# Kernel optimization log

Measured on AMD Instinct MI355X. Metric: run time of the kernel, lower is better.

The kernel has to match this reference:

```python
import jax, jax.numpy as jnp
import numpy as np

D = 100  # embedding_dim (hard-coded in the original module)


def _prelu(x, a):
    return jnp.where(x >= 0, x, a * x)


def setup_inputs() -> dict:
    key = jax.random.key(0)
    ks = jax.random.split(key, 12)
    B, S, L, R, V = 32, 50, 20, 16, 50000
    T = L * R  # tokens per sentence = len_max_sentence * n_routes
    return {
        "stories": jax.random.randint(ks[0], (B, S, T), 0, V),
        "queries": jax.random.randint(ks[1], (B, L), 0, V),
        "emb": 0.1 * jax.random.normal(ks[2], (V, D), dtype=jnp.float32),
        "in_mult": jnp.ones((T, D), dtype=jnp.float32),
        "q_mult": jnp.ones((L, D), dtype=jnp.float32),
        "keys": 0.1 * jax.random.normal(ks[3], (R, D), dtype=jnp.float32),
        "init_state": 0.1 * jax.random.normal(ks[4], (D,), dtype=jnp.float32),
        "U": 0.1 * jax.random.normal(ks[5], (R * D, D), dtype=jnp.float32),
        "Vw": 0.1 * jax.random.normal(ks[6], (R * D, R * D), dtype=jnp.float32),
        "Ww": 0.1 * jax.random.normal(ks[7], (R * D, R * D), dtype=jnp.float32),
        "Hw": 0.1 * jax.random.normal(ks[8], (D, D), dtype=jnp.float32),
        "Rw": 0.1 * jax.random.normal(ks[9], (V, D), dtype=jnp.float32),
        "alpha_in": jnp.ones((1,), dtype=jnp.float32),  # PReLU(init=1)
        "alpha_q": jnp.ones((1,), dtype=jnp.float32),
    }


def reference(stories, queries, emb, in_mult, q_mult, keys, init_state,
              U, Vw, Ww, Hw, Rw, alpha_in, alpha_q):
    B, S, T = stories.shape
    R = keys.shape[0]
    emb0 = emb.at[0].set(0.0)  # padding_idx=0 row is zero
    # stories -> [B,S,T,D] -> route-sum -> [B,S,R,D]
    x = emb0[stories] * in_mult
    x = x.reshape(B, S, R, T // R, D).sum(axis=3)
    # V(keys.flatten()) is constant across timesteps
    v_keys = (keys.reshape(-1) @ Vw.T).reshape(R, D)
    state0 = jnp.tile(init_state[None, None, :], (B, 1, 1))  # [B,1,D]

    def step(state, sent):  # state [B,1,D], sent [B,R,D]
        gate = jax.nn.sigmoid(sent * state + sent * keys)
        u = (state.reshape(B, D) @ U.T).reshape(B, R, D)
        w = (sent.reshape(B, R * D) @ Ww.T).reshape(B, R, D)
        cand = _prelu(u + v_keys + w, alpha_in)
        # null-sentence mask: zero out positions where gate == sigmoid(0) = 0.5
        mask = jax.lax.stop_gradient(jnp.where(gate == 0.5, 0.0, 1.0))
        state = state + (cand * gate * mask).sum(axis=1, keepdims=True)
        # torch.norm over singleton dim=1 (= elementwise abs), kept faithful
        state = state / jnp.sqrt(jnp.sum(state * state, axis=1, keepdims=True))
        return state, None

    state, _ = jax.lax.scan(step, state0, jnp.swapaxes(x, 0, 1))

    q = (emb0[queries] * q_mult).sum(axis=1, keepdims=True)  # [B,1,D]
    h = _prelu(q + (state.reshape(B, D) @ Hw.T).reshape(B, 1, D), alpha_q)
    return h.reshape(B, D) @ Rw.T  # [B, vocab]
```

## Files before the change

kernel.cpp:

```cpp
#include <hip/hip_runtime.h>
#include <cstddef>
#include <cstdint>

#define B_  32
#define S_  50
#define L_  20
#define R_  16
#define D_  100
#define V_  50000
#define T_  320
#define RD_ 1600
#define BS_ 1600
#define NG_ 25
#define NP_ 16

typedef float v4f __attribute__((ext_vector_type(4)));
typedef unsigned v2u __attribute__((ext_vector_type(2)));
typedef unsigned short u16;
#define NTL(p)  __builtin_nontemporal_load((const v4f*)(p))
#define NTL8(p) __builtin_nontemporal_load((const v2u*)(p))

__device__ __forceinline__ float uf(unsigned u) { return __uint_as_float(u); }

__device__ __forceinline__ void bsplit(float a, unsigned& h, unsigned& l) {
  const unsigned bits = __float_as_uint(a);
  const unsigned hb = bits & 0xffff0000u;
  h = hb >> 16;
  l = __float_as_uint(a - __uint_as_float(hb)) >> 16;
}

__global__ __launch_bounds__(512) void setup_kernel(
    const int* __restrict__ stories, const float* __restrict__ emb,
    const float* __restrict__ in_mult, const float* __restrict__ U,
    const float* __restrict__ Vw, const float* __restrict__ keys,
    const float* __restrict__ init_state, const float* __restrict__ Ww,
    u16* __restrict__ xh, u16* __restrict__ xl,
    u16* __restrict__ wh, u16* __restrict__ wl,
    float* __restrict__ table, float* __restrict__ vk, float* __restrict__ u0)
{
  const int blk = blockIdx.x, tid = threadIdx.x;
  if (blk < 1600) {
    __shared__ int toks[T_];
    const int* st = stories + (size_t)blk * T_;
    if (tid < T_) toks[tid] = st[tid];
    __syncthreads();
    if (tid < 400) {
      const int j4 = tid * 4;
      const int r  = j4 / D_;
      const int d4 = j4 - r * D_;
      float4 acc = make_float4(0.f, 0.f, 0.f, 0.f);
      #pragma unroll
      for (int l = 0; l < 20; ++l) {
        const int t = r * 20 + l;
        const int tok = toks[t];
        if (tok != 0) {
          float4 e = *(const float4*)&emb[(size_t)tok * D_ + d4];
          float4 m = *(const float4*)&in_mult[(size_t)t * D_ + d4];
          acc.x += e.x * m.x; acc.y += e.y * m.y;
          acc.z += e.z * m.z; acc.w += e.w * m.w;
        }
      }
      unsigned h0,h1,h2,h3,l0,l1,l2,l3;
      bsplit(acc.x, h0, l0); bsplit(acc.y, h1, l1);
      bsplit(acc.z, h2, l2); bsplit(acc.w, h3, l3);
      v2u hv, lv;
      hv.x = h0 | (h1 << 16); hv.y = h2 | (h3 << 16);
      lv.x = l0 | (l1 << 16); lv.y = l2 | (l3 << 16);
      *(v2u*)&xh[(size_t)blk * RD_ + j4] = hv;
      *(v2u*)&xl[(size_t)blk * RD_ + j4] = lv;
    }
  } else if (blk < 2000) {
    const int q = blk - 1600;
    const int g = q >> 4, p = q & 15;
    const float s0 = (p & 1) ? -1.f : 1.f;
    const float s1 = (p & 2) ? -1.f : 1.f;
    const float s2 = (p & 4) ? -1.f : 1.f;
    const float s3 = (p & 8) ? -1.f : 1.f;
    if (tid < 400) {
      const int j4 = tid * 4;
      float t[4];
      #pragma unroll
      for (int jj = 0; jj < 4; ++jj) {
        const float* ur = &U[(size_t)(j4 + jj) * D_ + 4 * g];
        t[jj] = s0*ur[0] + s1*ur[1] + s2*ur[2] + s3*ur[3];
      }
      *(float4*)&table[((size_t)(g * NP_ + p)) * RD_ + j4] =
          make_float4(t[0], t[1], t[2], t[3]);
    }
  } else if (blk < 2200) {
    const int wave = tid >> 6, lane = tid & 63;
    const int j = (blk - 2000) * 8 + wave;
    float acc = 0.f;
    for (int k = lane; k < RD_; k += 64)
      acc += keys[k] * Vw[(size_t)j * RD_ + k];
    #pragma unroll
    for (int off = 32; off > 0; off >>= 1) acc += __shfl_down(acc, off);
    if (lane == 0) vk[j] = acc;
  } else if (blk < 2400) {
    const int wave = tid >> 6, lane = tid & 63;
    const int j = (blk - 2200) * 8 + wave;
    const float* Ur = U + (size_t)j * D_;
    float acc = Ur[lane] * init_state[lane];
    if (lane < 36) acc += Ur[64 + lane] * init_state[64 + lane];
    #pragma unroll
    for (int off = 32; off > 0; off >>= 1) acc += __shfl_down(acc, off);
    if (lane == 0) u0[j] = acc;
  } else {
    const int e = ((blk - 2400) * 512 + tid) * 8;
    float4 a0 = *(const float4*)&Ww[e];
    float4 a1 = *(const float4*)&Ww[e + 4];
    unsigned h[8], l[8];
    bsplit(a0.x, h[0], l[0]); bsplit(a0.y, h[1], l[1]);
    bsplit(a0.z, h[2], l[2]); bsplit(a0.w, h[3], l[3]);
    bsplit(a1.x, h[4], l[4]); bsplit(a1.y, h[5], l[5]);
    bsplit(a1.z, h[6], l[6]); bsplit(a1.w, h[7], l[7]);
    uint4 hv = make_uint4(h[0]|(h[1]<<16), h[2]|(h[3]<<16),
                          h[4]|(h[5]<<16), h[6]|(h[7]<<16));
    uint4 lv = make_uint4(l[0]|(l[1]<<16), l[2]|(l[3]<<16),
                          l[4]|(l[5]<<16), l[6]|(l[7]<<16));
    *(uint4*)&wh[e] = hv;
    *(uint4*)&wl[e] = lv;
  }
}

typedef const __attribute__((address_space(1))) unsigned GAu;
typedef __attribute__((address_space(3))) unsigned LDSu;
#define GLL(SRC, DST) __builtin_amdgcn_global_load_lds((GAu*)(SRC), (LDSu*)(DST), 16, 0, 0)

__device__ __forceinline__ void mfma16(v4f& d, v4f a, v4f b) {
  asm("v_mfma_f32_16x16x32_bf16 %0, %1, %2, %0" : "+v"(d) : "v"(a), "v"(b));
}

__global__ __launch_bounds__(256) void gemm_mfma_kernel(
    const u16* __restrict__ xh, const u16* __restrict__ xl,
    const u16* __restrict__ wh, const u16* __restrict__ wl,
    float* __restrict__ C)
{
  __shared__ __align__(16) char smem[2][4][8192];
  const int tid = threadIdx.x;
  const int lane = tid & 63, wid = tid >> 6;
  const int bm = blockIdx.y * 128, bn = blockIdx.x * 128;

  int ldsoff[2], srcA[2], srcB[2];
  #pragma unroll
  for (int i = 0; i < 2; ++i) {
    const int chunk = wid * 2 + i;
    const int row = chunk * 16 + (lane >> 2);
    const int kb = (lane & 3) * 16;
    int ra = bm + row; if (ra > 1599) ra = 1599;
    int rb = bn + row; if (rb > 1599) rb = 1599;
    srcA[i] = ra * 3200 + kb;
    srcB[i] = rb * 3200 + kb;
    ldsoff[i] = chunk * 1024;
  }
  const char* gxh = (const char*)xh;
  const char* gxl = (const char*)xl;
  const char* gwh = (const char*)wh;
  const char* gwl = (const char*)wl;

  const int wm = wid >> 1, wn = wid & 1;
  const int r15 = lane & 15, q = lane >> 4;
  const int aoff = (wm * 64 + r15) * 64 + q * 16;
  const int boff = (wn * 64 + r15) * 64 + q * 16;

  v4f acc[4][4];
  #pragma unroll
  for (int i = 0; i < 4; ++i)
    #pragma unroll
    for (int j = 0; j < 4; ++j) acc[i][j] = (v4f)(0.f);

  auto stage = [&](int buf, int kt) {
    const int kb = kt * 64;
    #pragma unroll
    for (int i = 0; i < 2; ++i) {
      GLL(gxh + srcA[i] + kb, &smem[buf][0][ldsoff[i]]);
      GLL(gxl + srcA[i] + kb, &smem[buf][1][ldsoff[i]]);
      GLL(gwh + srcB[i] + kb, &smem[buf][2][ldsoff[i]]);
      GLL(gwl + srcB[i] + kb, &smem[buf][3][ldsoff[i]]);
    }
  };

  stage(0, 0);
  __syncthreads();

  for (int kt = 0; kt < 50; ++kt) {
    const int cur = kt & 1;
    if (kt < 49) stage(cur ^ 1, kt + 1);
    const char* s0 = &smem[cur][0][0];
    v4f ah[4], al[4], bh[4], bl[4];
    #pragma unroll
    for (int t = 0; t < 4; ++t) {
      ah[t] = *(const v4f*)(s0 +         aoff + t * 1024);
      al[t] = *(const v4f*)(s0 +  8192 + aoff + t * 1024);
      bh[t] = *(const v4f*)(s0 + 16384 + boff + t * 1024);
      bl[t] = *(const v4f*)(s0 + 24576 + boff + t * 1024);
    }
    #pragma unroll
    for (int im = 0; im < 4; ++im)
      #pragma unroll
      for (int in = 0; in < 4; ++in) {
        mfma16(acc[im][in], ah[im], bh[in]);
        mfma16(acc[im][in], ah[im], bl[in]);
        mfma16(acc[im][in], al[im], bh[in]);
      }
    __syncthreads();
  }

  const int mb  = bm + wm * 64 + q * 4;
  const int nbq = bn + wn * 64 + r15;
  #pragma unroll
  for (int im = 0; im < 4; ++im) {
    #pragma unroll
    for (int in = 0; in < 4; ++in) {
      const int n = nbq + in * 16;
      const int m0 = mb + im * 16;
      if (n < 1600) {
        #pragma unroll
        for (int r = 0; r < 4; ++r)
          if (m0 + r < 1600)
            C[(size_t)(m0 + r) * 1600 + n] = acc[im][in][r];
      }
    }
  }
}

__global__ __launch_bounds__(512, 2) void scan_kernel(
    const u16* __restrict__ xh,
    const u16* __restrict__ xl,
    const float* __restrict__ Wall,
    const float* __restrict__ table,
    const float* __restrict__ u0,
    const float* __restrict__ vkeys,
    const float* __restrict__ keys,
    const float* __restrict__ init_state,
    const float* __restrict__ alpha_in_p,
    const int*   __restrict__ queries,
    const float* __restrict__ emb,
    const float* __restrict__ q_mult,
    const float* __restrict__ Hw,
    const float* __restrict__ alpha_q_p,
    float* __restrict__ h_g)
{
  const int b = blockIdx.x, tid = threadIdx.x;
  __shared__ __align__(16) float s_state[D_];
  __shared__ __align__(16) float s_c[RD_];
  __shared__ float s_hw[D_ * 101];
  __shared__ unsigned long long s_mask[2];
  const float alpha = alpha_in_p[0];
  const bool active = (tid < 400);
  const int j4 = tid * 4;
  const int d4 = (j4 % D_);
  float4 kk = make_float4(0.f,0.f,0.f,0.f), vv = kk;
  const u16*   xhb = xh   + (size_t)b * S_ * RD_;
  const u16*   xlb = xl   + (size_t)b * S_ * RD_;
  const float* wb  = Wall + (size_t)b * S_ * RD_;
  v2u bxh[5], bxl[5]; v4f bw[5];
  #pragma unroll
  for (int i = 0; i < 5; ++i) { bxh[i] = (v2u)(0u); bxl[i] = (v2u)(0u); bw[i] = (v4f)(0.f); }
  if (active) {
    kk = *(const float4*)&keys[j4];
    vv = *(const float4*)&vkeys[j4];
    #pragma unroll
    for (int i = 0; i < 5; ++i) {
      bxh[i] = NTL8(&xhb[(size_t)i * RD_ + j4]);
      bxl[i] = NTL8(&xlb[(size_t)i * RD_ + j4]);
      bw[i]  = NTL(&wb[(size_t)i * RD_ + j4]);
    }
  }
  if (tid < D_) s_state[tid] = init_state[tid];
  __syncthreads();

  for (int sg = 0; sg < S_; sg += 5) {
    #pragma unroll
    for (int i = 0; i < 5; ++i) {
      const int s = sg + i;
      if (active) {
        const v2u hxv = bxh[i], lxv = bxl[i];
        const v4f w = bw[i];
        if (s + 5 < S_) {
          bxh[i] = NTL8(&xhb[(size_t)(s + 5) * RD_ + j4]);
          bxl[i] = NTL8(&xlb[(size_t)(s + 5) * RD_ + j4]);
          bw[i]  = NTL(&wb[(size_t)(s + 5) * RD_ + j4]);
        }
        v4f sent;
        sent.x = uf(hxv.x << 16)          + uf(lxv.x << 16);
        sent.y = uf(hxv.x & 0xffff0000u)  + uf(lxv.x & 0xffff0000u);
        sent.z = uf(hxv.y << 16)          + uf(lxv.y << 16);
        sent.w = uf(hxv.y & 0xffff0000u)  + uf(lxv.y & 0xffff0000u);
        v4f u;
        if (s == 0) {
          float4 t0 = *(const float4*)&u0[j4];
          u.x = t0.x; u.y = t0.y; u.z = t0.z; u.w = t0.w;
        } else {
          u = (v4f)(0.f);
          const unsigned long long m0 = s_mask[0];
          const unsigned long long m1 = s_mask[1];
          #pragma unroll
          for (int g = 0; g < NG_; ++g) {
            const unsigned idx = (g < 16)
                ? (unsigned)((m0 >> (4 * g)) & 15ull)
                : (unsigned)((m1 >> (4 * g - 64)) & 15ull);
            float4 tv = *(const float4*)&table[((size_t)(g * NP_) + idx) * RD_ + j4];
            u.x += tv.x; u.y += tv.y; u.z += tv.z; u.w += tv.w;
          }
        }
        float4 sd = *(const float4*)&s_state[d4];
        float zx = sent.x * sd.x + sent.x * kk.x;
        float zy = sent.y * sd.y + sent.y * kk.y;
        float zz = sent.z * sd.z + sent.z * kk.z;
        float zw = sent.w * sd.w + sent.w * kk.w;
        float gx = 1.0f / (1.0f + expf(-zx));
        float gy = 1.0f / (1.0f + expf(-zy));
        float gz = 1.0f / (1.0f + expf(-zz));
        float gw = 1.0f / (1.0f + expf(-zw));
        float cx = u.x + vv.x + w.x; cx = cx >= 0.f ? cx : alpha * cx;
        float cy = u.y + vv.y + w.y; cy = cy >= 0.f ? cy : alpha * cy;
        float cz = u.z + vv.z + w.z; cz = cz >= 0.f ? cz : alpha * cz;
        float cw = u.w + vv.w + w.w; cw = cw >= 0.f ? cw : alpha * cw;
        v4f cc;
        cc.x = (gx == 0.5f) ? 0.f : cx * gx;
        cc.y = (gy == 0.5f) ? 0.f : cy * gy;
        cc.z = (gz == 0.5f) ? 0.f : cz * gz;
        cc.w = (gw == 0.5f) ? 0.f : cw * gw;
        *(v4f*)&s_c[j4] = cc;
      }
      __syncthreads();
      if (tid < D_) {
        float csum = 0.f;
        #pragma unroll
        for (int r = 0; r < R_; ++r) csum += s_c[r * D_ + tid];
        float v = s_state[tid] + csum;
        v = v / sqrtf(v * v);
        s_state[tid] = v;
        unsigned long long mask = __ballot(v < 0.f);
        if ((tid & 63) == 0) s_mask[tid >> 6] = mask;
      }
      __syncthreads();
    }
  }

  for (int f = tid; f < D_ * D_; f += 512) {
    const int row = f / D_, col = f - row * D_;
    s_hw[row * 101 + col] = Hw[f];
  }
  __syncthreads();
  if (tid < D_) {
    float q = 0.f;
    #pragma unroll
    for (int l = 0; l < L_; ++l) {
      const int tok = queries[b * L_ + l];
      if (tok != 0) q += emb[(size_t)tok * D_ + tid] * q_mult[l * D_ + tid];
    }
    float a = 0.f;
    #pragma unroll 4
    for (int k = 0; k < D_; ++k) a += s_state[k] * s_hw[tid * 101 + k];
    float h = q + a;
    const float aq = alpha_q_p[0];
    h = h >= 0.f ? h : aq * h;
    h_g[(size_t)b * D_ + tid] = h;
  }
}

__global__ __launch_bounds__(256) void out_kernel(
    const float* __restrict__ h_g, const float* __restrict__ Rw, float* __restrict__ out)
{
  __shared__ __align__(16) float sh[B_ * D_];
  __shared__ __align__(16) float sr[32 * D_];
  int tid = threadIdx.x;
  int v0 = blockIdx.x * 32;
  for (int i = tid; i < B_ * D_; i += 256) sh[i] = h_g[i];
  int nrows = V_ - v0; if (nrows > 32) nrows = 32;
  for (int i = tid; i < nrows * D_; i += 256) sr[i] = Rw[(size_t)v0 * D_ + i];
  __syncthreads();
  const float4* sh4 = (const float4*)sh;
  const float4* sr4 = (const float4*)sr;
  int tv = (tid & 15) * 2;
  int tb = (tid >> 4) * 2;
  float a00 = 0.f, a01 = 0.f, a10 = 0.f, a11 = 0.f;
  #pragma unroll
  for (int kc = 0; kc < 25; ++kc) {
    float4 h0 = sh4[tb * 25 + kc];
    float4 h1 = sh4[(tb + 1) * 25 + kc];
    float4 r0 = sr4[tv * 25 + kc];
    float4 r1 = sr4[(tv + 1) * 25 + kc];
    a00 += h0.x*r0.x + h0.y*r0.y + h0.z*r0.z + h0.w*r0.w;
    a01 += h0.x*r1.x + h0.y*r1.y + h0.z*r1.z + h0.w*r1.w;
    a10 += h1.x*r0.x + h1.y*r0.y + h1.z*r0.z + h1.w*r0.w;
    a11 += h1.x*r1.x + h1.y*r1.y + h1.z*r1.z + h1.w*r1.w;
  }
  if (tv < nrows) {
    out[(size_t)tb * V_ + v0 + tv] = a00;
    out[(size_t)(tb + 1) * V_ + v0 + tv] = a10;
  }
  if (tv + 1 < nrows) {
    out[(size_t)tb * V_ + v0 + tv + 1] = a01;
    out[(size_t)(tb + 1) * V_ + v0 + tv + 1] = a11;
  }
}

extern "C" void kernel_launch(void* const* d_in, const int* in_sizes, int n_in,
                              void* d_out, int out_size, void* d_ws, size_t ws_size,
                              hipStream_t stream) {
  const int*   stories    = (const int*)  d_in[0];
  const int*   queries    = (const int*)  d_in[1];
  const float* emb        = (const float*)d_in[2];
  const float* in_mult    = (const float*)d_in[3];
  const float* q_mult     = (const float*)d_in[4];
  const float* keys       = (const float*)d_in[5];
  const float* init_state = (const float*)d_in[6];
  const float* U          = (const float*)d_in[7];
  const float* Vw         = (const float*)d_in[8];
  const float* Ww         = (const float*)d_in[9];
  const float* Hw         = (const float*)d_in[10];
  const float* Rw         = (const float*)d_in[11];
  const float* alpha_in   = (const float*)d_in[12];
  const float* alpha_q    = (const float*)d_in[13];
  float* out = (float*)d_out;

  char* ws = (char*)d_ws;
  u16*   xh    = (u16*)  (ws);
  u16*   xl    = (u16*)  (ws +  5120000);
  float* Wall  = (float*)(ws + 10240000);
  float* table = (float*)(ws + 20480000);
  u16*   wwh   = (u16*)  (ws + 23040000);
  u16*   wwl   = (u16*)  (ws + 28160000);
  float* vk    = (float*)(ws + 33280000);
  float* u0    = (float*)(ws + 33286400);
  float* hbuf  = (float*)(ws + 33292800);

  setup_kernel<<<3025, 512, 0, stream>>>(stories, emb, in_mult, U, Vw, keys,
                                         init_state, Ww, xh, xl, wwh, wwl,
                                         table, vk, u0);
  gemm_mfma_kernel<<<dim3(13, 13), 256, 0, stream>>>(xh, xl, wwh, wwl, Wall);
  scan_kernel<<<B_, 512, 0, stream>>>(xh, xl, Wall, table, u0, vk, keys,
                                      init_state, alpha_in, queries, emb,
                                      q_mult, Hw, alpha_q, hbuf);
  out_kernel<<<(V_ + 31) / 32, 256, 0, stream>>>(hbuf, Rw, out);
}
```

Before: 419.0 us.

## Store story sums as fp32 and split to bf16 hi/lo inside GEMM staging

The setup kernel now writes the route-summed story embeddings as plain fp32 instead of pre-split bf16 high/low arrays. The GEMM loads A through registers and does the bf16 split itself while filling shared memory, overlapping that with the MFMA work, and the scan kernel reads fp32 sentences directly with no reconstruction. This removes one workspace write and read pair and the unpack arithmetic in the serial scan, at the cost of register-path A staging in the GEMM in place of direct global-to-LDS loads.

```diff
diff --git a/kernel.cpp b/kernel.cpp
--- a/kernel.cpp
+++ b/kernel.cpp
@@ -15,10 +15,8 @@
 #define NP_ 16
 
 typedef float v4f __attribute__((ext_vector_type(4)));
-typedef unsigned v2u __attribute__((ext_vector_type(2)));
 typedef unsigned short u16;
 #define NTL(p)  __builtin_nontemporal_load((const v4f*)(p))
-#define NTL8(p) __builtin_nontemporal_load((const v2u*)(p))
 
 __device__ __forceinline__ float uf(unsigned u) { return __uint_as_float(u); }
 
@@ -29,12 +27,20 @@
   l = __float_as_uint(a - __uint_as_float(hb)) >> 16;
 }
 
+__device__ __forceinline__ void bsplit4(float4 a, uint2& h, uint2& l) {
+  unsigned h0,h1,h2,h3,l0,l1,l2,l3;
+  bsplit(a.x, h0, l0); bsplit(a.y, h1, l1);
+  bsplit(a.z, h2, l2); bsplit(a.w, h3, l3);
+  h.x = h0 | (h1 << 16); h.y = h2 | (h3 << 16);
+  l.x = l0 | (l1 << 16); l.y = l2 | (l3 << 16);
+}
+
 __global__ __launch_bounds__(512) void setup_kernel(
     const int* __restrict__ stories, const float* __restrict__ emb,
     const float* __restrict__ in_mult, const float* __restrict__ U,
     const float* __restrict__ Vw, const float* __restrict__ keys,
     const float* __restrict__ init_state, const float* __restrict__ Ww,
-    u16* __restrict__ xh, u16* __restrict__ xl,
+    float* __restrict__ x,
     u16* __restrict__ wh, u16* __restrict__ wl,
     float* __restrict__ table, float* __restrict__ vk, float* __restrict__ u0)
 {
@@ -60,14 +66,7 @@
           acc.z += e.z * m.z; acc.w += e.w * m.w;
         }
       }
-      unsigned h0,h1,h2,h3,l0,l1,l2,l3;
-      bsplit(acc.x, h0, l0); bsplit(acc.y, h1, l1);
-      bsplit(acc.z, h2, l2); bsplit(acc.w, h3, l3);
-      v2u hv, lv;
-      hv.x = h0 | (h1 << 16); hv.y = h2 | (h3 << 16);
-      lv.x = l0 | (l1 << 16); lv.y = l2 | (l3 << 16);
-      *(v2u*)&xh[(size_t)blk * RD_ + j4] = hv;
-      *(v2u*)&xl[(size_t)blk * RD_ + j4] = lv;
+      *(float4*)&x[(size_t)blk * RD_ + j4] = acc;
     }
   } else if (blk < 2000) {
     const int q = blk - 1600;
@@ -109,15 +108,11 @@
     const int e = ((blk - 2400) * 512 + tid) * 8;
     float4 a0 = *(const float4*)&Ww[e];
     float4 a1 = *(const float4*)&Ww[e + 4];
-    unsigned h[8], l[8];
-    bsplit(a0.x, h[0], l[0]); bsplit(a0.y, h[1], l[1]);
-    bsplit(a0.z, h[2], l[2]); bsplit(a0.w, h[3], l[3]);
-    bsplit(a1.x, h[4], l[4]); bsplit(a1.y, h[5], l[5]);
-    bsplit(a1.z, h[6], l[6]); bsplit(a1.w, h[7], l[7]);
-    uint4 hv = make_uint4(h[0]|(h[1]<<16), h[2]|(h[3]<<16),
-                          h[4]|(h[5]<<16), h[6]|(h[7]<<16));
-    uint4 lv = make_uint4(l[0]|(l[1]<<16), l[2]|(l[3]<<16),
-                          l[4]|(l[5]<<16), l[6]|(l[7]<<16));
+    uint2 h0, l0, h1, l1;
+    bsplit4(a0, h0, l0);
+    bsplit4(a1, h1, l1);
+    uint4 hv = make_uint4(h0.x, h0.y, h1.x, h1.y);
+    uint4 lv = make_uint4(l0.x, l0.y, l1.x, l1.y);
     *(uint4*)&wh[e] = hv;
     *(uint4*)&wl[e] = lv;
   }
@@ -132,7 +127,7 @@
 }
 
 __global__ __launch_bounds__(256) void gemm_mfma_kernel(
-    const u16* __restrict__ xh, const u16* __restrict__ xl,
+    const float* __restrict__ A,
     const u16* __restrict__ wh, const u16* __restrict__ wl,
     float* __restrict__ C)
 {
@@ -141,22 +136,28 @@
   const int lane = tid & 63, wid = tid >> 6;
   const int bm = blockIdx.y * 128, bn = blockIdx.x * 128;
 
-  int ldsoff[2], srcA[2], srcB[2];
+  int ldsoff[2], srcB[2];
   #pragma unroll
   for (int i = 0; i < 2; ++i) {
     const int chunk = wid * 2 + i;
     const int row = chunk * 16 + (lane >> 2);
     const int kb = (lane & 3) * 16;
-    int ra = bm + row; if (ra > 1599) ra = 1599;
     int rb = bn + row; if (rb > 1599) rb = 1599;
-    srcA[i] = ra * 3200 + kb;
     srcB[i] = rb * 3200 + kb;
     ldsoff[i] = chunk * 1024;
   }
-  const char* gxh = (const char*)xh;
-  const char* gxl = (const char*)xl;
   const char* gwh = (const char*)wh;
   const char* gwl = (const char*)wl;
+
+  int arow[4], awofs[4];
+  const int akseg = tid & 7;
+  #pragma unroll
+  for (int i = 0; i < 4; ++i) {
+    const int r = i * 32 + (tid >> 3);
+    int ra = bm + r; if (ra > 1599) ra = 1599;
+    arow[i] = ra;
+    awofs[i] = r * 64 + akseg * 8;
+  }
 
   const int wm = wid >> 1, wn = wid & 1;
   const int r15 = lane & 15, q = lane >> 4;
@@ -169,23 +170,37 @@
     #pragma unroll
     for (int j = 0; j < 4; ++j) acc[i][j] = (v4f)(0.f);
 
-  auto stage = [&](int buf, int kt) {
+  auto stageB = [&](int buf, int kt) {
     const int kb = kt * 64;
     #pragma unroll
     for (int i = 0; i < 2; ++i) {
-      GLL(gxh + srcA[i] + kb, &smem[buf][0][ldsoff[i]]);
-      GLL(gxl + srcA[i] + kb, &smem[buf][1][ldsoff[i]]);
       GLL(gwh + srcB[i] + kb, &smem[buf][2][ldsoff[i]]);
       GLL(gwl + srcB[i] + kb, &smem[buf][3][ldsoff[i]]);
     }
   };
 
-  stage(0, 0);
+  float4 a4[4];
+
+  #pragma unroll
+  for (int i = 0; i < 4; ++i)
+    a4[i] = *(const float4*)&A[(size_t)arow[i] * RD_ + akseg * 4];
+  stageB(0, 0);
+  #pragma unroll
+  for (int i = 0; i < 4; ++i) {
+    uint2 h, l; bsplit4(a4[i], h, l);
+    *(uint2*)&smem[0][0][awofs[i]] = h;
+    *(uint2*)&smem[0][1][awofs[i]] = l;
+  }
   __syncthreads();
 
   for (int kt = 0; kt < 50; ++kt) {
     const int cur = kt & 1;
-    if (kt < 49) stage(cur ^ 1, kt + 1);
+    if (kt < 49) {
+      stageB(cur ^ 1, kt + 1);
+      #pragma unroll
+      for (int i = 0; i < 4; ++i)
+        a4[i] = *(const float4*)&A[(size_t)arow[i] * RD_ + (kt + 1) * 32 + akseg * 4];
+    }
     const char* s0 = &smem[cur][0][0];
     v4f ah[4], al[4], bh[4], bl[4];
     #pragma unroll
@@ -203,6 +218,15 @@
         mfma16(acc[im][in], ah[im], bl[in]);
         mfma16(acc[im][in], al[im], bh[in]);
       }
+    if (kt < 49) {
+      const int nxt = cur ^ 1;
+      #pragma unroll
+      for (int i = 0; i < 4; ++i) {
+        uint2 h, l; bsplit4(a4[i], h, l);
+        *(uint2*)&smem[nxt][0][awofs[i]] = h;
+        *(uint2*)&smem[nxt][1][awofs[i]] = l;
+      }
+    }
     __syncthreads();
   }
 
@@ -218,15 +242,14 @@
         #pragma unroll
         for (int r = 0; r < 4; ++r)
           if (m0 + r < 1600)
-            C[(size_t)(m0 + r) * 1600 + n] = acc[im][in][r];
+            C[(size_t)(m0 + r) * RD_ + n] = acc[im][in][r];
       }
     }
   }
 }
 
 __global__ __launch_bounds__(512, 2) void scan_kernel(
-    const u16* __restrict__ xh,
-    const u16* __restrict__ xl,
+    const float* __restrict__ x,
     const float* __restrict__ Wall,
     const float* __restrict__ table,
     const float* __restrict__ u0,
@@ -251,20 +274,18 @@
   const int j4 = tid * 4;
   const int d4 = (j4 % D_);
   float4 kk = make_float4(0.f,0.f,0.f,0.f), vv = kk;
-  const u16*   xhb = xh   + (size_t)b * S_ * RD_;
-  const u16*   xlb = xl   + (size_t)b * S_ * RD_;
-  const float* wb  = Wall + (size_t)b * S_ * RD_;
-  v2u bxh[5], bxl[5]; v4f bw[5];
-  #pragma unroll
-  for (int i = 0; i < 5; ++i) { bxh[i] = (v2u)(0u); bxl[i] = (v2u)(0u); bw[i] = (v4f)(0.f); }
+  const float* xb = x    + (size_t)b * S_ * RD_;
+  const float* wb = Wall + (size_t)b * S_ * RD_;
+  v4f bx[5], bw[5];
+  #pragma unroll
+  for (int i = 0; i < 5; ++i) { bx[i] = (v4f)(0.f); bw[i] = (v4f)(0.f); }
   if (active) {
     kk = *(const float4*)&keys[j4];
     vv = *(const float4*)&vkeys[j4];
     #pragma unroll
     for (int i = 0; i < 5; ++i) {
-      bxh[i] = NTL8(&xhb[(size_t)i * RD_ + j4]);
-      bxl[i] = NTL8(&xlb[(size_t)i * RD_ + j4]);
-      bw[i]  = NTL(&wb[(size_t)i * RD_ + j4]);
+      bx[i] = NTL(&xb[(size_t)i * RD_ + j4]);
+      bw[i] = NTL(&wb[(size_t)i * RD_ + j4]);
     }
   }
   if (tid < D_) s_state[tid] = init_state[tid];
@@ -275,18 +296,11 @@
     for (int i = 0; i < 5; ++i) {
       const int s = sg + i;
       if (active) {
-        const v2u hxv = bxh[i], lxv = bxl[i];
-        const v4f w = bw[i];
+        const v4f sent = bx[i], w = bw[i];
         if (s + 5 < S_) {
-          bxh[i] = NTL8(&xhb[(size_t)(s + 5) * RD_ + j4]);
-          bxl[i] = NTL8(&xlb[(size_t)(s + 5) * RD_ + j4]);
-          bw[i]  = NTL(&wb[(size_t)(s + 5) * RD_ + j4]);
+          bx[i] = NTL(&xb[(size_t)(s + 5) * RD_ + j4]);
+          bw[i] = NTL(&wb[(size_t)(s + 5) * RD_ + j4]);
         }
-        v4f sent;
-        sent.x = uf(hxv.x << 16)          + uf(lxv.x << 16);
-        sent.y = uf(hxv.x & 0xffff0000u)  + uf(lxv.x & 0xffff0000u);
-        sent.z = uf(hxv.y << 16)          + uf(lxv.y << 16);
-        sent.w = uf(hxv.y & 0xffff0000u)  + uf(lxv.y & 0xffff0000u);
         v4f u;
         if (s == 0) {
           float4 t0 = *(const float4*)&u0[j4];
@@ -418,8 +432,7 @@
   float* out = (float*)d_out;
 
   char* ws = (char*)d_ws;
-  u16*   xh    = (u16*)  (ws);
-  u16*   xl    = (u16*)  (ws +  5120000);
+  float* x     = (float*)(ws);
   float* Wall  = (float*)(ws + 10240000);
   float* table = (float*)(ws + 20480000);
   u16*   wwh   = (u16*)  (ws + 23040000);
@@ -429,11 +442,11 @@
   float* hbuf  = (float*)(ws + 33292800);
 
   setup_kernel<<<3025, 512, 0, stream>>>(stories, emb, in_mult, U, Vw, keys,
-                                         init_state, Ww, xh, xl, wwh, wwl,
+                                         init_state, Ww, x, wwh, wwl,
                                          table, vk, u0);
-  gemm_mfma_kernel<<<dim3(13, 13), 256, 0, stream>>>(xh, xl, wwh, wwl, Wall);
-  scan_kernel<<<B_, 512, 0, stream>>>(xh, xl, Wall, table, u0, vk, keys,
-                                      init_state, alpha_in, queries, emb,
-                                      q_mult, Hw, alpha_q, hbuf);
+  gemm_mfma_kernel<<<dim3(13, 13), 256, 0, stream>>>(x, wwh, wwl, Wall);
+  scan_kernel<<<B_, 512, 0, stream>>>(x, Wall, table, u0, vk, keys, init_state,
+                                      alpha_in, queries, emb, q_mult, Hw, alpha_q,
+                                      hbuf);
   out_kernel<<<(V_ + 31) / 32, 256, 0, stream>>>(hbuf, Rw, out);
 }
```

After: 386.3 us. 1.08x faster.
